# Kernel optimization log

Hardware: AMD Instinct MI355X
Metric: run time of the kernel (lower is better)

The kernel has to match this reference:

```python
import jax, jax.numpy as jnp
import numpy as np

EMBED_DIM = 512
N_HEAD = 8
Q_DIM = 64
V_DIM = 64
WINDOW_SIZE = 3


def setup_inputs() -> dict:
    key = jax.random.key(0)
    ks = jax.random.split(key, 9)
    B, N = 2, 2048
    x = jax.random.normal(ks[0], (B, N, EMBED_DIM), dtype=jnp.float32)
    s = 0.02
    # torch nn.Linear weights are [out_features, in_features]; y = x @ W.T + b
    Wq = jax.random.normal(ks[1], (N_HEAD * Q_DIM, EMBED_DIM), dtype=jnp.float32) * s
    bq = jax.random.normal(ks[2], (N_HEAD * Q_DIM,), dtype=jnp.float32) * s
    Wk = jax.random.normal(ks[3], (N_HEAD * Q_DIM, EMBED_DIM), dtype=jnp.float32) * s
    bk = jax.random.normal(ks[4], (N_HEAD * Q_DIM,), dtype=jnp.float32) * s
    Wv = jax.random.normal(ks[5], (N_HEAD * V_DIM, EMBED_DIM), dtype=jnp.float32) * s
    bv = jax.random.normal(ks[6], (N_HEAD * V_DIM,), dtype=jnp.float32) * s
    Wo = jax.random.normal(ks[7], (EMBED_DIM, N_HEAD * V_DIM), dtype=jnp.float32) * s
    bo = jax.random.normal(ks[8], (EMBED_DIM,), dtype=jnp.float32) * s
    return {"x": x, "Wq": Wq, "bq": bq, "Wk": Wk, "bk": bk,
            "Wv": Wv, "bv": bv, "Wo": Wo, "bo": bo}


def _diag_indices(n_seq, di):
    # rows i and cols j = i + di of the di-th diagonal
    if di >= 0:
        ii = np.arange(0, n_seq - di)
    else:
        ii = np.arange(-di, n_seq)
    return ii, ii + di


def reference(x, Wq, bq, Wk, bk, Wv, bv, Wo, bo):
    B, N, E = x.shape
    H, Dq, Dv = N_HEAD, Q_DIM, V_DIM
    Q = (x @ Wq.T + bq).reshape(B, N, H, Dq).transpose(0, 2, 1, 3)  # [B,H,N,Dq]
    K = (x @ Wk.T + bk).reshape(B, N, H, Dq).transpose(0, 2, 1, 3)
    V = (x @ Wv.T + bv).reshape(B, N, H, Dv).transpose(0, 2, 1, 3)  # [B,H,N,Dv]
    half = WINDOW_SIZE // 2
    # Faithful to source: scores scattered into COLUMN index i (the loop
    # counter), not the key position; all other columns remain 0 and still
    # participate in the full softmax over n_seq.
    columns = jnp.zeros((B, H, N, N), dtype=x.dtype)
    for i, di in enumerate(range(-half, half + 1)):
        ii, jj = _diag_indices(N, di)
        c = jnp.einsum('bhid,bhid->bhi', Q[:, :, ii, :], K[:, :, jj, :])
        columns = columns.at[:, :, ii, i].set(c)
    attn = jax.nn.softmax(columns, axis=-1)          # [B,H,N,N]
    out = attn @ V                                    # [B,H,N,Dv]
    out = out.transpose(0, 2, 1, 3).reshape(B, N, H * Dv)
    return out @ Wo.T + bo
```

## Files before the change

### kernel.cpp

```cpp
#include <hip/hip_runtime.h>
#include <hip/hip_bf16.h>

#define EMBED 512
#define NSEQ 2048
#define NROWS 4096

typedef unsigned short u16;
typedef __bf16 bf16x8 __attribute__((ext_vector_type(8)));
typedef float f32x4 __attribute__((ext_vector_type(4)));
typedef unsigned short ushort8 __attribute__((ext_vector_type(8)));

__device__ __forceinline__ u16 f2bf(float f) {
    unsigned u = __float_as_uint(f);
    unsigned r = (u + 0x7FFFu + ((u >> 16) & 1u)) >> 16;
    return (u16)r;
}
__device__ __forceinline__ float bf2f(u16 v) {
    return __uint_as_float((unsigned)v << 16);
}

#define XELEMS    (NROWS * EMBED)
#define WQKELEMS  (1024 * EMBED)

__global__ __launch_bounds__(256) void prep_kernel(
    const float* __restrict__ x,
    const float* __restrict__ Wq, const float* __restrict__ Wk,
    u16* __restrict__ xb, u16* __restrict__ Wcat,
    float* __restrict__ xcs_part)
{
    __shared__ float cs[4][512];
    const int bid = blockIdx.x, t = threadIdx.x;
    if (bid < 256) {
        const float* src = x + (size_t)bid * 16 * EMBED;
        u16* dst = xb + (size_t)bid * 16 * EMBED;
        const int rl = t >> 6;
        const int co = (t & 63) * 8;
        float s0=0.f,s1=0.f,s2=0.f,s3=0.f,s4=0.f,s5=0.f,s6=0.f,s7=0.f;
#pragma unroll
        for (int i = 0; i < 4; ++i) {
            const size_t off = (size_t)(i * 4 + rl) * EMBED + co;
            float4 a = *(const float4*)(src + off);
            float4 b = *(const float4*)(src + off + 4);
            union { u16 u[8]; uint4 v; } p;
            p.u[0]=f2bf(a.x); p.u[1]=f2bf(a.y); p.u[2]=f2bf(a.z); p.u[3]=f2bf(a.w);
            p.u[4]=f2bf(b.x); p.u[5]=f2bf(b.y); p.u[6]=f2bf(b.z); p.u[7]=f2bf(b.w);
            *(uint4*)(dst + off) = p.v;
            s0+=a.x; s1+=a.y; s2+=a.z; s3+=a.w;
            s4+=b.x; s5+=b.y; s6+=b.z; s7+=b.w;
        }
        f32x4 v0 = {s0,s1,s2,s3}, v1 = {s4,s5,s6,s7};
        *(f32x4*)&cs[rl][co]     = v0;
        *(f32x4*)&cs[rl][co + 4] = v1;
        __syncthreads();
        const int b = bid >> 7, blk = bid & 127;
#pragma unroll
        for (int d = t; d < 512; d += 256) {
            xcs_part[((size_t)b * 512 + d) * 128 + blk] =
                cs[0][d] + cs[1][d] + cs[2][d] + cs[3][d];
        }
    } else {
        const long long e0 = (long long)(bid - 256) * 2048 + (long long)t * 8;
        const int row = (int)(e0 >> 9), col = (int)(e0 & 511);
        const float* src = (row < 512) ? (Wq + (size_t)row * EMBED + col)
                                       : (Wk + (size_t)(row - 512) * EMBED + col);
        float4 a = *(const float4*)(src);
        float4 b = *(const float4*)(src + 4);
        union { u16 u[8]; uint4 v; } p;
        p.u[0]=f2bf(a.x); p.u[1]=f2bf(a.y); p.u[2]=f2bf(a.z); p.u[3]=f2bf(a.w);
        p.u[4]=f2bf(b.x); p.u[5]=f2bf(b.y); p.u[6]=f2bf(b.z); p.u[7]=f2bf(b.w);
        *(uint4*)(Wcat + e0) = p.v;
    }
}

__global__ __launch_bounds__(256) void gemm_qk_mfma(
    const u16* __restrict__ A, const u16* __restrict__ W,
    const float* __restrict__ bq, const float* __restrict__ bk,
    const float* __restrict__ xcs_part, const float* __restrict__ bv,
    const float* __restrict__ Wv, const float* __restrict__ Wo,
    u16* __restrict__ QKb, float* __restrict__ WT)
{
    __shared__ __align__(16) u16 As[128 * 64];
    __shared__ __align__(16) u16 Bs[64 * 64];
    const int t = threadIdx.x;

    if (blockIdx.x >= 512) {
        float* xcs  = (float*)As;
        float* Vraw = (float*)Bs;
        float* Vloc = Vraw + 256;
        const int sid = blockIdx.x - 512;
        const int b = sid >> 4, h = (sid >> 1) & 7, jhalf = sid & 1;

        {
            const float* p = xcs_part + ((size_t)b * 512 + 2 * t) * 128;
            float a0 = 0.f, a1 = 0.f;
#pragma unroll 4
            for (int i = 0; i < 128; i += 4) {
                f32x4 u0 = *(const f32x4*)(p + i);
                f32x4 u1 = *(const f32x4*)(p + 128 + i);
                a0 += u0[0] + u0[1] + u0[2] + u0[3];
                a1 += u1[0] + u1[1] + u1[2] + u1[3];
            }
            xcs[2 * t] = a0; xcs[2 * t + 1] = a1;
        }
        __syncthreads();

        const int tt = t >> 6, cl = t & 63;
        const int col = h * 64 + cl;
        const float* wv = Wv + (size_t)col * EMBED;
        float r = 0.f;
        if (tt < 3) {
            const u16* xr = A + ((size_t)b * NSEQ + tt) * EMBED;
#pragma unroll 8
            for (int d = 0; d < EMBED; d += 8) {
                ushort8 xv = *(const ushort8*)(xr + d);
                f32x4 w0 = *(const f32x4*)(wv + d);
                f32x4 w1 = *(const f32x4*)(wv + d + 4);
                r = fmaf(bf2f(xv[0]), w0[0], r);
                r = fmaf(bf2f(xv[1]), w0[1], r);
                r = fmaf(bf2f(xv[2]), w0[2], r);
                r = fmaf(bf2f(xv[3]), w0[3], r);
                r = fmaf(bf2f(xv[4]), w1[0], r);
                r = fmaf(bf2f(xv[5]), w1[1], r);
                r = fmaf(bf2f(xv[6]), w1[2], r);
                r = fmaf(bf2f(xv[7]), w1[3], r);
            }
        } else {
#pragma unroll 8
            for (int d = 0; d < EMBED; d += 4) {
                f32x4 w = *(const f32x4*)(wv + d);
                r = fmaf(xcs[d],     w[0], r);
                r = fmaf(xcs[d + 1], w[1], r);
                r = fmaf(xcs[d + 2], w[2], r);
                r = fmaf(xcs[d + 3], w[3], r);
            }
        }
        Vraw[tt * 64 + cl] = r;
        __syncthreads();
        const float bvc = bv[col];
        if (tt < 3) Vloc[tt * 64 + cl] = r + bvc;
        else        Vloc[192 + cl] = r - (Vraw[cl] + Vraw[64 + cl] + Vraw[128 + cl])
                                       + 2045.f * bvc;
        __syncthreads();

        const int j = jhalf * 256 + t;
        const float* wo = Wo + (size_t)j * EMBED + h * 64;
        float a0 = 0.f, a1 = 0.f, a2 = 0.f, a3 = 0.f;
#pragma unroll
        for (int c = 0; c < 64; c += 4) {
            f32x4 w = *(const f32x4*)(wo + c);
#pragma unroll
            for (int z = 0; z < 4; ++z) {
                a0 = fmaf(Vloc[c + z],       w[z], a0);
                a1 = fmaf(Vloc[64 + c + z],  w[z], a1);
                a2 = fmaf(Vloc[128 + c + z], w[z], a2);
                a3 = fmaf(Vloc[192 + c + z], w[z], a3);
            }
        }
        float* wt = WT + ((size_t)b * 512 + j) * 32 + h * 4;
        wt[0] = a0; wt[1] = a1; wt[2] = a2; wt[3] = a3;
        return;
    }

    const int m0 = (blockIdx.x & 31) * 128;
    const int n0 = (blockIdx.x >> 5) * 64;
    const int sel = n0 >> 9;
    const float* bias = ((sel == 0) ? bq : bk) + (n0 & 511);

    const int wave = t >> 6, lane = t & 63;
    const int wm   = wave >> 1, wn = wave & 1;
    const int qd   = lane >> 4, lr = lane & 15;

    const int sr8 = lane >> 3;
    const int sg  = (lane & 7) ^ sr8;
    const int soff = sg * 8;

    f32x4 acc[4][2] = {};

    const u16* Ag = A + (size_t)m0 * EMBED;
    const u16* Wg = W + (size_t)n0 * EMBED;

    u16* Adst = As + (size_t)(wave * 8) * 64;
    u16* Bdst = Bs + (size_t)(wave * 8) * 64;
    const u16* Asrc = Ag + (size_t)(wave * 8 + sr8) * EMBED + soff;
    const u16* Bsrc = Wg + (size_t)(wave * 8 + sr8) * EMBED + soff;

    for (int kc = 0; kc < EMBED; kc += 64) {
#pragma unroll
        for (int j = 0; j < 4; ++j)
            __builtin_amdgcn_global_load_lds(
                (const __attribute__((address_space(1))) void*)(Asrc + kc + (size_t)j * 32 * EMBED),
                (__attribute__((address_space(3))) void*)(Adst + j * 32 * 64), 16, 0, 0);
#pragma unroll
        for (int j = 0; j < 2; ++j)
            __builtin_amdgcn_global_load_lds(
                (const __attribute__((address_space(1))) void*)(Bsrc + kc + (size_t)j * 32 * EMBED),
                (__attribute__((address_space(3))) void*)(Bdst + j * 32 * 64), 16, 0, 0);
        __syncthreads();

#pragma unroll
        for (int kk = 0; kk < 2; ++kk) {
            const int gr = ((kk * 4 + qd) ^ (lr & 7)) * 8;
            bf16x8 af[4], bfr[2];
#pragma unroll
            for (int i = 0; i < 4; ++i)
                af[i]  = *(const bf16x8*)&As[(wm * 64 + i * 16 + lr) * 64 + gr];
#pragma unroll
            for (int i = 0; i < 2; ++i)
                bfr[i] = *(const bf16x8*)&Bs[(wn * 32 + i * 16 + lr) * 64 + gr];
#pragma unroll
            for (int mi = 0; mi < 4; ++mi)
#pragma unroll
                for (int ni = 0; ni < 2; ++ni)
                    acc[mi][ni] = __builtin_amdgcn_mfma_f32_16x16x32_bf16(
                        af[mi], bfr[ni], acc[mi][ni], 0, 0, 0);
        }
        __syncthreads();
    }

#pragma unroll
    for (int ni = 0; ni < 2; ++ni) {
        const int cl = wn * 32 + ni * 16 + lr;
        const float bb = bias[cl];
#pragma unroll
        for (int mi = 0; mi < 4; ++mi)
#pragma unroll
            for (int e = 0; e < 4; ++e) {
                const int row = m0 + wm * 64 + mi * 16 + qd * 4 + e;
                QKb[(size_t)row * 1024 + n0 + cl] = f2bf(acc[mi][ni][e] + bb);
            }
    }
}

__global__ __launch_bounds__(256) void attn_out_kernel(
    const u16* __restrict__ QKb, const float* __restrict__ WT,
    const float* __restrict__ bo, float* __restrict__ out)
{
    __shared__ float E[8][32];
    const int r0   = blockIdx.x * 8;
    const int b    = r0 >> 11;
    const int wave = threadIdx.x >> 6, lane = threadIdx.x & 63;
    const int d0   = lane * 8;

#pragma unroll
    for (int i = 0; i < 2; ++i) {
        const int rl = wave * 2 + i;
        const int r  = r0 + rl;
        const int sr = r & (NSEQ - 1);
        const u16* Qr = QKb + (size_t)r * 1024 + d0;
        const u16* Kr = QKb + (size_t)r * 1024 + 512 + d0;

        ushort8 qv = *(const ushort8*)Qr;
        ushort8 kv = *(const ushort8*)Kr;
        float q[8], k[8];
#pragma unroll
        for (int z = 0; z < 8; ++z) { q[z] = bf2f(qv[z]); k[z] = bf2f(kv[z]); }

        float s1 = 0.f;
#pragma unroll
        for (int z = 0; z < 8; ++z) s1 = fmaf(q[z], k[z], s1);

        float s0 = 0.f, s2 = 0.f;
        if (sr > 0) {
            ushort8 pv = *(const ushort8*)(Kr - 1024);
#pragma unroll
            for (int z = 0; z < 8; ++z) s0 = fmaf(q[z], bf2f(pv[z]), s0);
        }
        if (sr < NSEQ - 1) {
            ushort8 nv = *(const ushort8*)(Kr + 1024);
#pragma unroll
            for (int z = 0; z < 8; ++z) s2 = fmaf(q[z], bf2f(nv[z]), s2);
        }
#pragma unroll
        for (int off = 1; off <= 4; off <<= 1) {
            s0 += __shfl_xor(s0, off);
            s1 += __shfl_xor(s1, off);
            s2 += __shfl_xor(s2, off);
        }
        const float m  = fmaxf(fmaxf(s0, s1), fmaxf(s2, 0.f));
        const float e0 = __expf(s0 - m);
        const float e1 = __expf(s1 - m);
        const float e2 = __expf(s2 - m);
        const float eb = __expf(-m);
        const float rd = 1.f / (e0 + e1 + e2 + (float)(NSEQ - 3) * eb);
        const int h = lane >> 3, jj = lane & 7;
        const float coef = (jj == 0) ? e0 : (jj == 1) ? e1 : (jj == 2) ? e2 : eb;
        if (jj < 4) E[rl][h * 4 + jj] = coef * rd;
    }
    __syncthreads();

    const int j0 = threadIdx.x * 2;
    const float* WTb = WT + (size_t)b * 512 * 32;
    float w0[32], w1[32];
#pragma unroll
    for (int s = 0; s < 32; ++s) {
        w0[s] = WTb[(size_t)j0 * 32 + s];
        w1[s] = WTb[(size_t)(j0 + 1) * 32 + s];
    }
    const float b0 = bo[j0], b1 = bo[j0 + 1];
#pragma unroll
    for (int rl = 0; rl < 8; ++rl) {
        float a0 = b0, a1 = b1;
#pragma unroll
        for (int s = 0; s < 32; ++s) {
            const float e = E[rl][s];
            a0 = fmaf(e, w0[s], a0);
            a1 = fmaf(e, w1[s], a1);
        }
        *(float2*)(out + (size_t)(r0 + rl) * EMBED + j0) = make_float2(a0, a1);
    }
}

extern "C" void kernel_launch(void* const* d_in, const int* in_sizes, int n_in,
                              void* d_out, int out_size, void* d_ws, size_t ws_size,
                              hipStream_t stream)
{
    const float* x  = (const float*)d_in[0];
    const float* Wq = (const float*)d_in[1];
    const float* bq = (const float*)d_in[2];
    const float* Wk = (const float*)d_in[3];
    const float* bk = (const float*)d_in[4];
    const float* Wv = (const float*)d_in[5];
    const float* bv = (const float*)d_in[6];
    const float* Wo = (const float*)d_in[7];
    const float* bo = (const float*)d_in[8];
    float* out = (float*)d_out;

    u16*   QKb      = (u16*)d_ws;
    u16*   xb       = QKb + (size_t)NROWS * 1024;
    u16*   Wcat     = xb + XELEMS;
    float* xcs_part = (float*)(Wcat + WQKELEMS);
    float* WT       = xcs_part + 2 * 512 * 128;

    prep_kernel<<<512, 256, 0, stream>>>(x, Wq, Wk, xb, Wcat, xcs_part);
    gemm_qk_mfma<<<544, 256, 0, stream>>>(xb, Wcat, bq, bk, xcs_part, bv, Wv, Wo,
                                          QKb, WT);
    attn_out_kernel<<<512, 256, 0, stream>>>(QKb, WT, bo, out);
}
```

Before: 126.1 us.

## Double-buffer QK GEMM, transpose column-sum partials, reorder blocks, enlarge attention row tiles

The QK GEMM now double-buffers its LDS tiles, issuing the next k-chunk's global-to-LDS loads before computing the current one so load latency overlaps MFMA work. The WT-building side blocks move to the front of the grid so they are scheduled first. The column-sum partials are stored row-major per block, which gives coalesced writes and contiguous reads in the reducer. The attention/output kernel handles 16 rows per block instead of 8, reusing the per-thread WT register loads over more rows at the cost of fewer blocks and more LDS use for the GEMM.

```diff
diff --git a/kernel.cpp b/kernel.cpp
--- a/kernel.cpp
+++ b/kernel.cpp
@@ -55,7 +55,7 @@
         const int b = bid >> 7, blk = bid & 127;
 #pragma unroll
         for (int d = t; d < 512; d += 256) {
-            xcs_part[((size_t)b * 512 + d) * 128 + blk] =
+            xcs_part[((size_t)b * 128 + blk) * 512 + d] =
                 cs[0][d] + cs[1][d] + cs[2][d] + cs[3][d];
         }
     } else {
@@ -79,28 +79,27 @@
     const float* __restrict__ Wv, const float* __restrict__ Wo,
     u16* __restrict__ QKb, float* __restrict__ WT)
 {
-    __shared__ __align__(16) u16 As[128 * 64];
-    __shared__ __align__(16) u16 Bs[64 * 64];
+    __shared__ __align__(16) u16 As[2 * 128 * 64];
+    __shared__ __align__(16) u16 Bs[2 * 64 * 64];
     const int t = threadIdx.x;
 
-    if (blockIdx.x >= 512) {
+    if (blockIdx.x < 32) {
         float* xcs  = (float*)As;
         float* Vraw = (float*)Bs;
         float* Vloc = Vraw + 256;
-        const int sid = blockIdx.x - 512;
+        const int sid = blockIdx.x;
         const int b = sid >> 4, h = (sid >> 1) & 7, jhalf = sid & 1;
 
         {
-            const float* p = xcs_part + ((size_t)b * 512 + 2 * t) * 128;
-            float a0 = 0.f, a1 = 0.f;
+            const float* p = xcs_part + (size_t)b * 128 * 512 + 2 * t;
+            float a0 = 0.f, a1 = 0.f, c0 = 0.f, c1 = 0.f;
 #pragma unroll 4
-            for (int i = 0; i < 128; i += 4) {
-                f32x4 u0 = *(const f32x4*)(p + i);
-                f32x4 u1 = *(const f32x4*)(p + 128 + i);
-                a0 += u0[0] + u0[1] + u0[2] + u0[3];
-                a1 += u1[0] + u1[1] + u1[2] + u1[3];
-            }
-            xcs[2 * t] = a0; xcs[2 * t + 1] = a1;
+            for (int blk = 0; blk < 128; blk += 2) {
+                float2 u = *(const float2*)(p + (size_t)blk * 512);
+                float2 v = *(const float2*)(p + (size_t)(blk + 1) * 512);
+                a0 += u.x; a1 += u.y; c0 += v.x; c1 += v.y;
+            }
+            xcs[2 * t] = a0 + c0; xcs[2 * t + 1] = a1 + c1;
         }
         __syncthreads();
 
@@ -161,8 +160,9 @@
         return;
     }
 
-    const int m0 = (blockIdx.x & 31) * 128;
-    const int n0 = (blockIdx.x >> 5) * 64;
+    const int bb = blockIdx.x - 32;
+    const int m0 = (bb & 31) * 128;
+    const int n0 = (bb >> 5) * 64;
     const int sel = n0 >> 9;
     const float* bias = ((sel == 0) ? bq : bk) + (n0 & 511);
 
@@ -176,37 +176,48 @@
 
     f32x4 acc[4][2] = {};
 
-    const u16* Ag = A + (size_t)m0 * EMBED;
-    const u16* Wg = W + (size_t)n0 * EMBED;
-
-    u16* Adst = As + (size_t)(wave * 8) * 64;
-    u16* Bdst = Bs + (size_t)(wave * 8) * 64;
-    const u16* Asrc = Ag + (size_t)(wave * 8 + sr8) * EMBED + soff;
-    const u16* Bsrc = Wg + (size_t)(wave * 8 + sr8) * EMBED + soff;
-
-    for (int kc = 0; kc < EMBED; kc += 64) {
-#pragma unroll
-        for (int j = 0; j < 4; ++j)
-            __builtin_amdgcn_global_load_lds(
-                (const __attribute__((address_space(1))) void*)(Asrc + kc + (size_t)j * 32 * EMBED),
-                (__attribute__((address_space(3))) void*)(Adst + j * 32 * 64), 16, 0, 0);
-#pragma unroll
-        for (int j = 0; j < 2; ++j)
-            __builtin_amdgcn_global_load_lds(
-                (const __attribute__((address_space(1))) void*)(Bsrc + kc + (size_t)j * 32 * EMBED),
-                (__attribute__((address_space(3))) void*)(Bdst + j * 32 * 64), 16, 0, 0);
-        __syncthreads();
-
+    const u16* Asrc = A + (size_t)m0 * EMBED + (size_t)(wave * 8 + sr8) * EMBED + soff;
+    const u16* Bsrc = W + (size_t)n0 * EMBED + (size_t)(wave * 8 + sr8) * EMBED + soff;
+
+    u16* Ad0 = As + (size_t)(wave * 8) * 64;
+    u16* Bd0 = Bs + (size_t)(wave * 8) * 64;
+
+#define STAGE(bufi, kc)                                                          \
+    do {                                                                         \
+        u16* Ad = Ad0 + (bufi) * (128 * 64);                                     \
+        u16* Bd = Bd0 + (bufi) * (64 * 64);                                      \
+        _Pragma("unroll")                                                        \
+        for (int j = 0; j < 4; ++j)                                              \
+            __builtin_amdgcn_global_load_lds(                                    \
+                (const __attribute__((address_space(1))) void*)(Asrc + (kc) + (size_t)j * 32 * EMBED), \
+                (__attribute__((address_space(3))) void*)(Ad + j * 32 * 64), 16, 0, 0); \
+        _Pragma("unroll")                                                        \
+        for (int j = 0; j < 2; ++j)                                              \
+            __builtin_amdgcn_global_load_lds(                                    \
+                (const __attribute__((address_space(1))) void*)(Bsrc + (kc) + (size_t)j * 32 * EMBED), \
+                (__attribute__((address_space(3))) void*)(Bd + j * 32 * 64), 16, 0, 0); \
+    } while (0)
+
+    STAGE(0, 0);
+    __syncthreads();
+
+    int cur = 0;
+#pragma unroll
+    for (int ki = 0; ki < 8; ++ki) {
+        if (ki < 7) STAGE(cur ^ 1, (ki + 1) * 64);
+
+        const u16* Ab = As + cur * (128 * 64);
+        const u16* Bb = Bs + cur * (64 * 64);
 #pragma unroll
         for (int kk = 0; kk < 2; ++kk) {
             const int gr = ((kk * 4 + qd) ^ (lr & 7)) * 8;
             bf16x8 af[4], bfr[2];
 #pragma unroll
             for (int i = 0; i < 4; ++i)
-                af[i]  = *(const bf16x8*)&As[(wm * 64 + i * 16 + lr) * 64 + gr];
+                af[i]  = *(const bf16x8*)&Ab[(wm * 64 + i * 16 + lr) * 64 + gr];
 #pragma unroll
             for (int i = 0; i < 2; ++i)
-                bfr[i] = *(const bf16x8*)&Bs[(wn * 32 + i * 16 + lr) * 64 + gr];
+                bfr[i] = *(const bf16x8*)&Bb[(wn * 32 + i * 16 + lr) * 64 + gr];
 #pragma unroll
             for (int mi = 0; mi < 4; ++mi)
 #pragma unroll
@@ -214,19 +225,21 @@
                     acc[mi][ni] = __builtin_amdgcn_mfma_f32_16x16x32_bf16(
                         af[mi], bfr[ni], acc[mi][ni], 0, 0, 0);
         }
-        __syncthreads();
-    }
+        if (ki < 7) __syncthreads();
+        cur ^= 1;
+    }
+#undef STAGE
 
 #pragma unroll
     for (int ni = 0; ni < 2; ++ni) {
         const int cl = wn * 32 + ni * 16 + lr;
-        const float bb = bias[cl];
+        const float bb2 = bias[cl];
 #pragma unroll
         for (int mi = 0; mi < 4; ++mi)
 #pragma unroll
             for (int e = 0; e < 4; ++e) {
                 const int row = m0 + wm * 64 + mi * 16 + qd * 4 + e;
-                QKb[(size_t)row * 1024 + n0 + cl] = f2bf(acc[mi][ni][e] + bb);
+                QKb[(size_t)row * 1024 + n0 + cl] = f2bf(acc[mi][ni][e] + bb2);
             }
     }
 }
@@ -235,15 +248,15 @@
     const u16* __restrict__ QKb, const float* __restrict__ WT,
     const float* __restrict__ bo, float* __restrict__ out)
 {
-    __shared__ float E[8][32];
-    const int r0   = blockIdx.x * 8;
+    __shared__ float E[16][32];
+    const int r0   = blockIdx.x * 16;
     const int b    = r0 >> 11;
     const int wave = threadIdx.x >> 6, lane = threadIdx.x & 63;
     const int d0   = lane * 8;
 
 #pragma unroll
-    for (int i = 0; i < 2; ++i) {
-        const int rl = wave * 2 + i;
+    for (int i = 0; i < 4; ++i) {
+        const int rl = wave * 4 + i;
         const int r  = r0 + rl;
         const int sr = r & (NSEQ - 1);
         const u16* Qr = QKb + (size_t)r * 1024 + d0;
@@ -298,7 +311,7 @@
     }
     const float b0 = bo[j0], b1 = bo[j0 + 1];
 #pragma unroll
-    for (int rl = 0; rl < 8; ++rl) {
+    for (int rl = 0; rl < 16; ++rl) {
         float a0 = b0, a1 = b1;
 #pragma unroll
         for (int s = 0; s < 32; ++s) {
@@ -329,10 +342,10 @@
     u16*   xb       = QKb + (size_t)NROWS * 1024;
     u16*   Wcat     = xb + XELEMS;
     float* xcs_part = (float*)(Wcat + WQKELEMS);
-    float* WT       = xcs_part + 2 * 512 * 128;
+    float* WT       = xcs_part + 2 * 128 * 512;
 
     prep_kernel<<<512, 256, 0, stream>>>(x, Wq, Wk, xb, Wcat, xcs_part);
     gemm_qk_mfma<<<544, 256, 0, stream>>>(xb, Wcat, bq, bk, xcs_part, bv, Wv, Wo,
                                           QKb, WT);
-    attn_out_kernel<<<512, 256, 0, stream>>>(QKb, WT, bo, out);
-}
+    attn_out_kernel<<<256, 256, 0, stream>>>(QKb, WT, bo, out);
+}
```

Result: faster. 117.6 us (-6.7%).
